# Optimization experiments

Measured on AMD Instinct MI355X. Metric: run time of the kernel, lower is better.

The kernel has to match this reference:

```python
import jax, jax.numpy as jnp
import numpy as np

BITS = 4
QMAX = (1 << BITS) - 1      # 15
QHALF = 1 << (BITS - 1)     # 8
B, S = 4, 2048
IN, OUT, FP = 4096, 4096, 256
INT = IN - FP


def setup_inputs() -> dict:
    key = jax.random.key(0)
    k0, k1, k2, k3 = jax.random.split(key, 4)
    x = jax.random.normal(k0, (B, S, IN), dtype=jnp.float16)
    # disjoint outlier / int feature index sets (QUIK splits columns by outlier-ness)
    perm = np.random.default_rng(0).permutation(IN)
    fp_indices = jnp.sort(jnp.asarray(perm[:FP], dtype=jnp.int32))
    int_indices = jnp.sort(jnp.asarray(perm[FP:], dtype=jnp.int32))
    # unpacked int4 weight values in [-8, 7] (torch stores these packed 2-per-uint8)
    int_weight = jax.random.randint(k1, (OUT, INT), -QHALF, QHALF, dtype=jnp.int8)
    weights_scales = (jax.random.uniform(k2, (OUT, 1), dtype=jnp.float32) * 0.01 + 1e-3).astype(jnp.float16)
    fp_weight = (jax.random.normal(k3, (OUT, FP), dtype=jnp.float32) * 0.02).astype(jnp.float16)
    bias = jnp.zeros((OUT,), dtype=jnp.float16)
    # reduced_w[j] = w_scale[j] * sum_k int_weight[j, k]  (precomputed zero-point correction)
    reduced_w = (weights_scales.astype(jnp.float32)[:, 0] * jnp.sum(int_weight.astype(jnp.float32), axis=1)).reshape(1, OUT).astype(jnp.float16)
    return {"x": x, "int_weight": int_weight, "fp_weight": fp_weight, "bias": bias,
            "weights_scales": weights_scales, "reduced_w": reduced_w,
            "int_indices": int_indices, "fp_indices": fp_indices}


def reference(x, int_weight, fp_weight, bias, weights_scales, reduced_w, int_indices, fp_indices):
    b, s, in_feat = x.shape
    xf = x.reshape(-1, in_feat)                       # [N, in] tokens
    int_x = xf[:, int_indices].astype(jnp.float32)    # [N, INT]
    fp_x = xf[:, fp_indices].astype(jnp.float32)      # [N, FP] outliers stay fp16-precision
    # asymmetric per-token quantization (quik.asymmetric.quantize)
    mn = jnp.min(int_x, axis=1, keepdims=True)
    mx = jnp.max(int_x, axis=1, keepdims=True)
    scale = jnp.maximum((mx - mn) / QMAX, 1e-8)       # [N,1]
    q = (jnp.clip(jnp.round((int_x - mn) / scale), 0, QMAX) - QHALF).astype(jnp.int8)  # signed int4 in [-8,7]
    zero = scale * QHALF + mn                         # [N,1] shifted zero point
    # int4 GEMM (quik.matmul.int4Matmul), int32 accumulate
    int_res = jnp.einsum('nk,ok->no', q, int_weight, preferred_element_type=jnp.int32)
    # fp outlier branch fused with bias (F.linear)
    fp_res = fp_x @ fp_weight.astype(jnp.float32).T + bias.astype(jnp.float32)[None, :]
    # quik.asymmetric.dequantize: q*scale_x*scale_w + zero_x*reduced_w + fp_result
    out = (int_res.astype(jnp.float32) * scale * weights_scales.astype(jnp.float32)[:, 0][None, :]
           + zero * reduced_w.astype(jnp.float32) + fp_res)
    return out.astype(jnp.float16).reshape(b, s, -1)
```

## Files before the change

kernel.cpp:

```cpp
#include <hip/hip_runtime.h>
#include <hip/hip_bf16.h>
#include <stdint.h>

#define N_TOK 8192
#define IN_F  4096
#define OUT_F 4096
#define FP_F  256
#define INT_F 3840
#define PROW  1920

typedef int    v4i   __attribute__((ext_vector_type(4)));
typedef int    v16i  __attribute__((ext_vector_type(16)));
typedef float  v16f  __attribute__((ext_vector_type(16)));
typedef __bf16 bf16x8 __attribute__((ext_vector_type(8)));

#define WS_QP   0u
#define WS_WP   15728640u
#define WS_FPX  23592960u
#define WS_WFP  27787264u
#define WS_F1   29884416u
#define WS_F2   29917184u
#define WS_F3   29949952u
#define WS_NEED 29982720u


__global__ __launch_bounds__(256) void zero_out_kernel(uint4* __restrict__ o) {
  o[(size_t)blockIdx.x * 256 + threadIdx.x] = uint4{0, 0, 0, 0};
}

__global__ __launch_bounds__(256) void pack_w_kernel(
    const int* __restrict__ w, uint8_t* __restrict__ wp) {
  int gid = blockIdx.x * 256 + threadIdx.x;
  int r = gid / 120, t = gid % 120;
  const int* src = w + (size_t)r * INT_F + t * 32;
  uint32_t u[4];
#pragma unroll
  for (int h = 0; h < 2; h++) {
    uint32_t a0 = 0, a1 = 0;
#pragma unroll
    for (int j = 0; j < 4; j++) {
      uint32_t lo0 = (uint32_t)(src[h * 16 + j] + 8) & 0xFu;
      uint32_t hi0 = (uint32_t)(src[h * 16 + 8 + j] + 8) & 0xFu;
      a0 |= (lo0 | (hi0 << 4)) << (8 * j);
      uint32_t lo1 = (uint32_t)(src[h * 16 + 4 + j] + 8) & 0xFu;
      uint32_t hi1 = (uint32_t)(src[h * 16 + 12 + j] + 8) & 0xFu;
      a1 |= (lo1 | (hi1 << 4)) << (8 * j);
    }
    u[h * 2] = a0; u[h * 2 + 1] = a1;
  }
  uint4 o4; o4.x = u[0]; o4.y = u[1]; o4.z = u[2]; o4.w = u[3];
  *(uint4*)(wp + (size_t)r * PROW + t * 16) = o4;
}

__global__ __launch_bounds__(256) void conv_wfp_kernel(
    const float* __restrict__ w, __hip_bfloat16* __restrict__ o) {
  int i = (blockIdx.x * 256 + threadIdx.x) * 4;
  float4 v = *(const float4*)(w + i);
  __hip_bfloat16 b[4] = {__float2bfloat16(v.x), __float2bfloat16(v.y),
                         __float2bfloat16(v.z), __float2bfloat16(v.w)};
  *(uint2*)(o + i) = *(const uint2*)b;
}

__global__ __launch_bounds__(256) void quant_kernel(
    const float* __restrict__ x,
    const int* __restrict__ int_idx, const int* __restrict__ fp_idx,
    uint8_t* __restrict__ qp, __hip_bfloat16* __restrict__ fpx,
    float* __restrict__ f1, float* __restrict__ f2, float* __restrict__ f3) {
  __shared__ float gath[INT_F];
  __shared__ float smn[4], smx[4], ssum[4];
  __shared__ float s_mn, s_sc;

  int n = blockIdx.x, tid = threadIdx.x;
  const float* xr = x + (size_t)n * IN_F;

  float lmn = 1e30f, lmx = -1e30f;
#pragma unroll
  for (int k = 0; k < 15; k++) {
    int i = tid + k * 256;
    float v = xr[int_idx[i]];
    int b = i >> 2;
    gath[(b ^ ((b >> 2) & 7)) * 4 + (i & 3)] = v;
    lmn = fminf(lmn, v);
    lmx = fmaxf(lmx, v);
  }
  fpx[(size_t)n * FP_F + tid] = __float2bfloat16(xr[fp_idx[tid]]);

#pragma unroll
  for (int off = 32; off > 0; off >>= 1) {
    lmn = fminf(lmn, __shfl_xor(lmn, off, 64));
    lmx = fmaxf(lmx, __shfl_xor(lmx, off, 64));
  }
  int wv = tid >> 6, ln = tid & 63;
  if (ln == 0) { smn[wv] = lmn; smx[wv] = lmx; }
  __syncthreads();
  if (tid == 0) {
    float mn = fminf(fminf(smn[0], smn[1]), fminf(smn[2], smn[3]));
    float mx = fmaxf(fmaxf(smx[0], smx[1]), fmaxf(smx[2], smx[3]));
    float sc = fmaxf((mx - mn) / 15.0f, 1e-8f);
    s_mn = mn; s_sc = sc;
    f1[n] = sc; f3[n] = mn;
  }
  __syncthreads();
  float mn = s_mn, sc = s_sc;

  float lsum = 0.0f;
  if (tid < 240) {
    int g = tid;
    const float4* g4 = (const float4*)gath;
    float4 q0 = g4[(g * 4 + 0) ^ (g & 7)];
    float4 q1 = g4[(g * 4 + 1) ^ (g & 7)];
    float4 q2 = g4[(g * 4 + 2) ^ (g & 7)];
    float4 q3 = g4[(g * 4 + 3) ^ (g & 7)];
    float vals[16] = {q0.x, q0.y, q0.z, q0.w, q1.x, q1.y, q1.z, q1.w,
                      q2.x, q2.y, q2.z, q2.w, q3.x, q3.y, q3.z, q3.w};
    uint32_t u0 = 0, u1 = 0;
#pragma unroll
    for (int i = 0; i < 4; i++) {
      float cA = fminf(fmaxf(rintf((vals[i] - mn) / sc), 0.0f), 15.0f);
      float cB = fminf(fmaxf(rintf((vals[i + 8] - mn) / sc), 0.0f), 15.0f);
      float cC = fminf(fmaxf(rintf((vals[i + 4] - mn) / sc), 0.0f), 15.0f);
      float cD = fminf(fmaxf(rintf((vals[i + 12] - mn) / sc), 0.0f), 15.0f);
      lsum += (cA + cB) + (cC + cD);
      u0 |= ((uint32_t)cA | ((uint32_t)cB << 4)) << (8 * i);
      u1 |= ((uint32_t)cC | ((uint32_t)cD << 4)) << (8 * i);
    }
    uint2 o2; o2.x = u0; o2.y = u1;
    *(uint2*)(qp + (size_t)n * PROW + g * 8) = o2;
  }
#pragma unroll
  for (int off = 32; off > 0; off >>= 1) lsum += __shfl_xor(lsum, off, 64);
  if (ln == 0) ssum[wv] = lsum;
  __syncthreads();
  if (tid == 0)
    f2[n] = -8.0f * (ssum[0] + ssum[1] + ssum[2] + ssum[3]) * s_sc;
}

__device__ inline v4i unpack_nib(uint2 u) {
  v4i r;
  r[0] = (int)(u.x & 0x0F0F0F0Fu);
  r[1] = (int)(u.y & 0x0F0F0F0Fu);
  r[2] = (int)((u.x >> 4) & 0x0F0F0F0Fu);
  r[3] = (int)((u.y >> 4) & 0x0F0F0F0Fu);
  return r;
}

__global__ __launch_bounds__(256, 4) void gemm_kernel(
    const uint8_t* __restrict__ qp, const uint8_t* __restrict__ wp,
    const __hip_bfloat16* __restrict__ fpx, const __hip_bfloat16* __restrict__ wfp,
    const float* __restrict__ f1, const float* __restrict__ f2,
    const float* __restrict__ f3,
    const float* __restrict__ wscale, const float* __restrict__ reduced,
    const float* __restrict__ bias, float* __restrict__ out) {
  __shared__ int4 lds4[1024];
  int8_t* lds = (int8_t*)lds4;

  int tid = threadIdx.x;
  int wave = tid >> 6, lane = tid & 63;
  int wm = wave >> 1, wn = wave & 1;
  int blk = blockIdx.x;
  int tileM = ((blk & 7) << 3) | ((blk >> 3) & 7);
  int tileN = blk >> 6;
  int n0 = tileM * 128, o0 = tileN * 128;

  union { v16i i; v16f f; } acc[2][2];
#pragma unroll
  for (int mi = 0; mi < 2; mi++)
#pragma unroll
    for (int ni = 0; ni < 2; ni++)
#pragma unroll
      for (int e = 0; e < 16; e++) acc[mi][ni].i[e] = 0;

  int m = lane & 31, kg = lane >> 5;
  int swm = (m & 3) ^ ((m >> 2) & 3);
  int sr = tid >> 1, sh = tid & 1;
  int swr = (sr & 3) ^ ((sr >> 2) & 3);
  uint32_t wa0 = (uint32_t)(sr * 4 + ((sh * 2) ^ swr)) * 8;
  uint32_t wa1 = (uint32_t)(sr * 4 + ((sh * 2 + 1) ^ swr)) * 8;
  const uint8_t* ga = qp + (size_t)(n0 + sr) * PROW + sh * 16;
  const uint8_t* gb = wp + (size_t)(o0 + sr) * PROW + sh * 16;

  uint4 pa = *(const uint4*)ga;
  uint4 pb = *(const uint4*)gb;
  for (int kt = 0; kt < 60; kt++) {
    {
      uint2 t0; t0.x = pa.x; t0.y = pa.y;
      uint2 t1; t1.x = pa.z; t1.y = pa.w;
      *(uint2*)&lds[wa0] = t0;
      *(uint2*)&lds[wa1] = t1;
      uint2 t2; t2.x = pb.x; t2.y = pb.y;
      uint2 t3; t3.x = pb.z; t3.y = pb.w;
      *(uint2*)&lds[4096 + wa0] = t2;
      *(uint2*)&lds[4096 + wa1] = t3;
    }
    __syncthreads();
    if (kt < 59) {
      pa = *(const uint4*)(ga + (kt + 1) * 32);
      pb = *(const uint4*)(gb + (kt + 1) * 32);
    }
#pragma unroll
    for (int ks = 0; ks < 2; ks++) {
      int slot = (ks * 2 + kg) ^ swm;
      v4i a[2], b[2];
#pragma unroll
      for (int mi = 0; mi < 2; mi++) {
        int row = wm * 64 + mi * 32 + m;
        a[mi] = unpack_nib(*(const uint2*)&lds[row * 32 + slot * 8]);
      }
#pragma unroll
      for (int ni = 0; ni < 2; ni++) {
        int row = wn * 64 + ni * 32 + m;
        b[ni] = unpack_nib(*(const uint2*)&lds[4096 + row * 32 + slot * 8]);
      }
#pragma unroll
      for (int mi = 0; mi < 2; mi++)
#pragma unroll
        for (int ni = 0; ni < 2; ni++)
          acc[mi][ni].i = __builtin_amdgcn_mfma_i32_32x32x32_i8(
              a[mi], b[ni], acc[mi][ni].i, 0, 0, 0);
    }
    __syncthreads();
  }

  int col = lane & 31, rb4 = (lane >> 5) * 4;
  float cws[2], crw[2], cbs[2];
#pragma unroll
  for (int ni = 0; ni < 2; ni++) {
    int o = o0 + wn * 64 + ni * 32 + col;
    cws[ni] = wscale[o]; crw[ni] = reduced[o]; cbs[ni] = bias[o];
  }
#pragma unroll
  for (int mi = 0; mi < 2; mi++) {
#pragma unroll
    for (int reg = 0; reg < 16; reg++) {
      int row = (reg & 3) + 8 * (reg >> 2) + rb4;
      int n = n0 + wm * 64 + mi * 32 + row;
      float a1 = f1[n], a2 = f2[n], a3 = f3[n];
      float d0 = (float)acc[mi][0].i[reg];
      float d1 = (float)acc[mi][1].i[reg];
      acc[mi][0].f[reg] = (d0 * a1 + a2) * cws[0] + a3 * crw[0] + cbs[0];
      acc[mi][1].f[reg] = (d1 * a1 + a2) * cws[1] + a3 * crw[1] + cbs[1];
    }
  }

  const int8_t* fpxb = (const int8_t*)fpx;
  const int8_t* fpwb = (const int8_t*)wfp;
  for (int kt = 0; kt < 8; kt++) {
#pragma unroll
    for (int i = 0; i < 2; i++) {
      int c = tid + i * 256;
      int r = c >> 2, s = c & 3;
      int ss = s ^ (r & 3) ^ ((r >> 2) & 3);
      *(int4*)&lds[(r * 4 + ss) * 16] =
          *(const int4*)(fpxb + (size_t)(n0 + r) * 512 + kt * 64 + s * 16);
    }
#pragma unroll
    for (int i = 0; i < 2; i++) {
      int c = tid + i * 256;
      int r = c >> 2, s = c & 3;
      int ss = s ^ (r & 3) ^ ((r >> 2) & 3);
      *(int4*)&lds[8192 + (r * 4 + ss) * 16] =
          *(const int4*)(fpwb + (size_t)(o0 + r) * 512 + kt * 64 + s * 16);
    }
    __syncthreads();
#pragma unroll
    for (int ks = 0; ks < 2; ks++) {
      bf16x8 a[2], b[2];
#pragma unroll
      for (int mi = 0; mi < 2; mi++) {
        int row = wm * 64 + mi * 32 + m;
        int seg = (ks * 2 + kg) ^ (row & 3) ^ ((row >> 2) & 3);
        a[mi] = *(const bf16x8*)&lds[(row * 4 + seg) * 16];
      }
#pragma unroll
      for (int ni = 0; ni < 2; ni++) {
        int row = wn * 64 + ni * 32 + m;
        int seg = (ks * 2 + kg) ^ (row & 3) ^ ((row >> 2) & 3);
        b[ni] = *(const bf16x8*)&lds[8192 + (row * 4 + seg) * 16];
      }
#pragma unroll
      for (int mi = 0; mi < 2; mi++)
#pragma unroll
        for (int ni = 0; ni < 2; ni++)
          acc[mi][ni].f = __builtin_amdgcn_mfma_f32_32x32x16_bf16(
              a[mi], b[ni], acc[mi][ni].f, 0, 0, 0);
    }
    __syncthreads();
  }

#pragma unroll
  for (int mi = 0; mi < 2; mi++) {
#pragma unroll
    for (int ni = 0; ni < 2; ni++) {
      int o = o0 + wn * 64 + ni * 32 + col;
#pragma unroll
      for (int reg = 0; reg < 16; reg++) {
        int row = (reg & 3) + 8 * (reg >> 2) + rb4;
        int n = n0 + wm * 64 + mi * 32 + row;
        out[(size_t)n * OUT_F + o] = acc[mi][ni].f[reg];
      }
    }
  }
}

extern "C" void kernel_launch(void* const* d_in, const int* in_sizes, int n_in,
                              void* d_out, int out_size, void* d_ws, size_t ws_size,
                              hipStream_t stream) {
  const float* x     = (const float*)d_in[0];
  const int*   int_w = (const int*)d_in[1];
  const float* fp_w  = (const float*)d_in[2];
  const float* bias  = (const float*)d_in[3];
  const float* wsc   = (const float*)d_in[4];
  const float* red   = (const float*)d_in[5];
  const int*   iidx  = (const int*)d_in[6];
  const int*   fidx  = (const int*)d_in[7];
  float*       out   = (float*)d_out;

  if (ws_size < (size_t)WS_NEED) {
    zero_out_kernel<<<out_size / 1024, 256, 0, stream>>>((uint4*)d_out);
    return;
  }

  uint8_t* ws = (uint8_t*)d_ws;
  uint8_t*        qp  = ws + WS_QP;
  uint8_t*        wpk = ws + WS_WP;
  __hip_bfloat16* fpx = (__hip_bfloat16*)(ws + WS_FPX);
  __hip_bfloat16* wfp = (__hip_bfloat16*)(ws + WS_WFP);
  float*          f1  = (float*)(ws + WS_F1);
  float*          f2  = (float*)(ws + WS_F2);
  float*          f3  = (float*)(ws + WS_F3);

  pack_w_kernel<<<OUT_F * 120 / 256, 256, 0, stream>>>(int_w, wpk);
  conv_wfp_kernel<<<OUT_F * FP_F / 4 / 256, 256, 0, stream>>>(fp_w, wfp);
  quant_kernel<<<N_TOK, 256, 0, stream>>>(x, iidx, fidx, qp, fpx, f1, f2, f3);
  gemm_kernel<<<(N_TOK / 128) * (OUT_F / 128), 256, 0, stream>>>(
      qp, wpk, fpx, wfp, f1, f2, f3, wsc, red, bias, out);
}
```

Measured before the change: 442.2 us.

## Double GEMM K-tile depth, coalesce weight packing, quantize in registers

The int4 GEMM main loop now stages 64 bytes of K per tile instead of 32, which halves the number of iterations and barriers. The fp outlier loop likewise moves 128-byte bf16 chunks, using a new XOR swizzle and twice the LDS. To fit the larger LDS footprint, launch bounds drop from 4 to 3 blocks per SM. The weight packing kernel now reads with vector int4 loads, one 32-bit output per thread. The quant kernel keeps the gathered values in registers, multiplies by a reciprocal instead of dividing, and packs nibbles through shuffles into a small LDS buffer before a coalesced store.

Result: faster. 414.7 us (-6.2%).

```diff
diff --git a/kernel.cpp b/kernel.cpp
--- a/kernel.cpp
+++ b/kernel.cpp
@@ -30,26 +30,16 @@
 
 __global__ __launch_bounds__(256) void pack_w_kernel(
     const int* __restrict__ w, uint8_t* __restrict__ wp) {
-  int gid = blockIdx.x * 256 + threadIdx.x;
-  int r = gid / 120, t = gid % 120;
-  const int* src = w + (size_t)r * INT_F + t * 32;
-  uint32_t u[4];
-#pragma unroll
-  for (int h = 0; h < 2; h++) {
-    uint32_t a0 = 0, a1 = 0;
-#pragma unroll
-    for (int j = 0; j < 4; j++) {
-      uint32_t lo0 = (uint32_t)(src[h * 16 + j] + 8) & 0xFu;
-      uint32_t hi0 = (uint32_t)(src[h * 16 + 8 + j] + 8) & 0xFu;
-      a0 |= (lo0 | (hi0 << 4)) << (8 * j);
-      uint32_t lo1 = (uint32_t)(src[h * 16 + 4 + j] + 8) & 0xFu;
-      uint32_t hi1 = (uint32_t)(src[h * 16 + 12 + j] + 8) & 0xFu;
-      a1 |= (lo1 | (hi1 << 4)) << (8 * j);
-    }
-    u[h * 2] = a0; u[h * 2 + 1] = a1;
-  }
-  uint4 o4; o4.x = u[0]; o4.y = u[1]; o4.z = u[2]; o4.w = u[3];
-  *(uint4*)(wp + (size_t)r * PROW + t * 16) = o4;
+  int t = blockIdx.x * 256 + threadIdx.x;
+  int r = t / 480, u = t % 480;
+  const int* src = w + (size_t)r * INT_F + (u >> 1) * 16 + (u & 1) * 4;
+  int4 lo = *(const int4*)src;
+  int4 hi = *(const int4*)(src + 8);
+  uint32_t o = (uint32_t)((lo.x + 8) & 15) | (uint32_t)((hi.x + 8) & 15) << 4 |
+               (uint32_t)((lo.y + 8) & 15) << 8 | (uint32_t)((hi.y + 8) & 15) << 12 |
+               (uint32_t)((lo.z + 8) & 15) << 16 | (uint32_t)((hi.z + 8) & 15) << 20 |
+               (uint32_t)((lo.w + 8) & 15) << 24 | (uint32_t)((hi.w + 8) & 15) << 28;
+  ((uint32_t*)wp)[t] = o;
 }
 
 __global__ __launch_bounds__(256) void conv_wfp_kernel(
@@ -66,22 +56,20 @@
     const int* __restrict__ int_idx, const int* __restrict__ fp_idx,
     uint8_t* __restrict__ qp, __hip_bfloat16* __restrict__ fpx,
     float* __restrict__ f1, float* __restrict__ f2, float* __restrict__ f3) {
-  __shared__ float gath[INT_F];
+  __shared__ uint2 qb[240];
   __shared__ float smn[4], smx[4], ssum[4];
-  __shared__ float s_mn, s_sc;
+  __shared__ float s_mn, s_inv, s_sc;
 
   int n = blockIdx.x, tid = threadIdx.x;
   const float* xr = x + (size_t)n * IN_F;
 
+  float v[15];
   float lmn = 1e30f, lmx = -1e30f;
 #pragma unroll
   for (int k = 0; k < 15; k++) {
-    int i = tid + k * 256;
-    float v = xr[int_idx[i]];
-    int b = i >> 2;
-    gath[(b ^ ((b >> 2) & 7)) * 4 + (i & 3)] = v;
-    lmn = fminf(lmn, v);
-    lmx = fmaxf(lmx, v);
+    v[k] = xr[int_idx[tid + 256 * k]];
+    lmn = fminf(lmn, v[k]);
+    lmx = fmaxf(lmx, v[k]);
   }
   fpx[(size_t)n * FP_F + tid] = __float2bfloat16(xr[fp_idx[tid]]);
 
@@ -97,35 +85,23 @@
     float mn = fminf(fminf(smn[0], smn[1]), fminf(smn[2], smn[3]));
     float mx = fmaxf(fmaxf(smx[0], smx[1]), fmaxf(smx[2], smx[3]));
     float sc = fmaxf((mx - mn) / 15.0f, 1e-8f);
-    s_mn = mn; s_sc = sc;
+    s_mn = mn; s_sc = sc; s_inv = 1.0f / sc;
     f1[n] = sc; f3[n] = mn;
   }
   __syncthreads();
-  float mn = s_mn, sc = s_sc;
-
+  float mn = s_mn, inv = s_inv;
+
+  uint8_t* qbb = (uint8_t*)qb;
   float lsum = 0.0f;
-  if (tid < 240) {
-    int g = tid;
-    const float4* g4 = (const float4*)gath;
-    float4 q0 = g4[(g * 4 + 0) ^ (g & 7)];
-    float4 q1 = g4[(g * 4 + 1) ^ (g & 7)];
-    float4 q2 = g4[(g * 4 + 2) ^ (g & 7)];
-    float4 q3 = g4[(g * 4 + 3) ^ (g & 7)];
-    float vals[16] = {q0.x, q0.y, q0.z, q0.w, q1.x, q1.y, q1.z, q1.w,
-                      q2.x, q2.y, q2.z, q2.w, q3.x, q3.y, q3.z, q3.w};
-    uint32_t u0 = 0, u1 = 0;
-#pragma unroll
-    for (int i = 0; i < 4; i++) {
-      float cA = fminf(fmaxf(rintf((vals[i] - mn) / sc), 0.0f), 15.0f);
-      float cB = fminf(fmaxf(rintf((vals[i + 8] - mn) / sc), 0.0f), 15.0f);
-      float cC = fminf(fmaxf(rintf((vals[i + 4] - mn) / sc), 0.0f), 15.0f);
-      float cD = fminf(fmaxf(rintf((vals[i + 12] - mn) / sc), 0.0f), 15.0f);
-      lsum += (cA + cB) + (cC + cD);
-      u0 |= ((uint32_t)cA | ((uint32_t)cB << 4)) << (8 * i);
-      u1 |= ((uint32_t)cC | ((uint32_t)cD << 4)) << (8 * i);
-    }
-    uint2 o2; o2.x = u0; o2.y = u1;
-    *(uint2*)(qp + (size_t)n * PROW + g * 8) = o2;
+#pragma unroll
+  for (int k = 0; k < 15; k++) {
+    float c = fminf(fmaxf(rintf((v[k] - mn) * inv), 0.0f), 15.0f);
+    lsum += c;
+    float ch = __shfl_down(c, 8, 64);
+    if ((tid & 15) < 8) {
+      qbb[(tid >> 4) * 8 + (tid & 7) + 128 * k] =
+          (uint8_t)((uint32_t)c | ((uint32_t)ch << 4));
+    }
   }
 #pragma unroll
   for (int off = 32; off > 0; off >>= 1) lsum += __shfl_xor(lsum, off, 64);
@@ -133,6 +109,8 @@
   __syncthreads();
   if (tid == 0)
     f2[n] = -8.0f * (ssum[0] + ssum[1] + ssum[2] + ssum[3]) * s_sc;
+  if (tid < 240)
+    *(uint2*)(qp + (size_t)n * PROW + tid * 8) = qb[tid];
 }
 
 __device__ inline v4i unpack_nib(uint2 u) {
@@ -144,14 +122,14 @@
   return r;
 }
 
-__global__ __launch_bounds__(256, 4) void gemm_kernel(
+__global__ __launch_bounds__(256, 3) void gemm_kernel(
     const uint8_t* __restrict__ qp, const uint8_t* __restrict__ wp,
     const __hip_bfloat16* __restrict__ fpx, const __hip_bfloat16* __restrict__ wfp,
     const float* __restrict__ f1, const float* __restrict__ f2,
     const float* __restrict__ f3,
     const float* __restrict__ wscale, const float* __restrict__ reduced,
     const float* __restrict__ bias, float* __restrict__ out) {
-  __shared__ int4 lds4[1024];
+  __shared__ int4 lds4[2048];
   int8_t* lds = (int8_t*)lds4;
 
   int tid = threadIdx.x;
@@ -171,45 +149,50 @@
       for (int e = 0; e < 16; e++) acc[mi][ni].i[e] = 0;
 
   int m = lane & 31, kg = lane >> 5;
-  int swm = (m & 3) ^ ((m >> 2) & 3);
-  int sr = tid >> 1, sh = tid & 1;
-  int swr = (sr & 3) ^ ((sr >> 2) & 3);
-  uint32_t wa0 = (uint32_t)(sr * 4 + ((sh * 2) ^ swr)) * 8;
-  uint32_t wa1 = (uint32_t)(sr * 4 + ((sh * 2 + 1) ^ swr)) * 8;
-  const uint8_t* ga = qp + (size_t)(n0 + sr) * PROW + sh * 16;
-  const uint8_t* gb = wp + (size_t)(o0 + sr) * PROW + sh * 16;
-
-  uint4 pa = *(const uint4*)ga;
-  uint4 pb = *(const uint4*)gb;
-  for (int kt = 0; kt < 60; kt++) {
+
+  int sra = tid >> 2, s16i = tid & 3;
+  const uint8_t* ga0 = qp + (size_t)(n0 + sra) * PROW + s16i * 16;
+  const uint8_t* ga1 = qp + (size_t)(n0 + sra + 64) * PROW + s16i * 16;
+  const uint8_t* gb0 = wp + (size_t)(o0 + sra) * PROW + s16i * 16;
+  const uint8_t* gb1 = wp + (size_t)(o0 + sra + 64) * PROW + s16i * 16;
+  uint32_t aw00 = sra * 64 + (((s16i * 2)     ^ ((sra >> 1) & 7)) * 8);
+  uint32_t aw01 = sra * 64 + (((s16i * 2 + 1) ^ ((sra >> 1) & 7)) * 8);
+  uint32_t aw10 = (sra + 64) * 64 + (((s16i * 2)     ^ (((sra + 64) >> 1) & 7)) * 8);
+  uint32_t aw11 = (sra + 64) * 64 + (((s16i * 2 + 1) ^ (((sra + 64) >> 1) & 7)) * 8);
+
+  uint4 pa0 = *(const uint4*)ga0, pa1 = *(const uint4*)ga1;
+  uint4 pb0 = *(const uint4*)gb0, pb1 = *(const uint4*)gb1;
+  for (int kt = 0; kt < 30; kt++) {
     {
-      uint2 t0; t0.x = pa.x; t0.y = pa.y;
-      uint2 t1; t1.x = pa.z; t1.y = pa.w;
-      *(uint2*)&lds[wa0] = t0;
-      *(uint2*)&lds[wa1] = t1;
-      uint2 t2; t2.x = pb.x; t2.y = pb.y;
-      uint2 t3; t3.x = pb.z; t3.y = pb.w;
-      *(uint2*)&lds[4096 + wa0] = t2;
-      *(uint2*)&lds[4096 + wa1] = t3;
+      uint2 t0; t0.x = pa0.x; t0.y = pa0.y; *(uint2*)&lds[aw00] = t0;
+      uint2 t1; t1.x = pa0.z; t1.y = pa0.w; *(uint2*)&lds[aw01] = t1;
+      uint2 t2; t2.x = pa1.x; t2.y = pa1.y; *(uint2*)&lds[aw10] = t2;
+      uint2 t3; t3.x = pa1.z; t3.y = pa1.w; *(uint2*)&lds[aw11] = t3;
+      uint2 t4; t4.x = pb0.x; t4.y = pb0.y; *(uint2*)&lds[8192 + aw00] = t4;
+      uint2 t5; t5.x = pb0.z; t5.y = pb0.w; *(uint2*)&lds[8192 + aw01] = t5;
+      uint2 t6; t6.x = pb1.x; t6.y = pb1.y; *(uint2*)&lds[8192 + aw10] = t6;
+      uint2 t7; t7.x = pb1.z; t7.y = pb1.w; *(uint2*)&lds[8192 + aw11] = t7;
     }
     __syncthreads();
-    if (kt < 59) {
-      pa = *(const uint4*)(ga + (kt + 1) * 32);
-      pb = *(const uint4*)(gb + (kt + 1) * 32);
-    }
-#pragma unroll
-    for (int ks = 0; ks < 2; ks++) {
-      int slot = (ks * 2 + kg) ^ swm;
+    if (kt < 29) {
+      pa0 = *(const uint4*)(ga0 + (kt + 1) * 64);
+      pa1 = *(const uint4*)(ga1 + (kt + 1) * 64);
+      pb0 = *(const uint4*)(gb0 + (kt + 1) * 64);
+      pb1 = *(const uint4*)(gb1 + (kt + 1) * 64);
+    }
+#pragma unroll
+    for (int ks = 0; ks < 4; ks++) {
+      int s8 = ks * 2 + kg;
       v4i a[2], b[2];
 #pragma unroll
       for (int mi = 0; mi < 2; mi++) {
         int row = wm * 64 + mi * 32 + m;
-        a[mi] = unpack_nib(*(const uint2*)&lds[row * 32 + slot * 8]);
+        a[mi] = unpack_nib(*(const uint2*)&lds[row * 64 + ((s8 ^ ((row >> 1) & 7)) * 8)]);
       }
 #pragma unroll
       for (int ni = 0; ni < 2; ni++) {
         int row = wn * 64 + ni * 32 + m;
-        b[ni] = unpack_nib(*(const uint2*)&lds[4096 + row * 32 + slot * 8]);
+        b[ni] = unpack_nib(*(const uint2*)&lds[8192 + row * 64 + ((s8 ^ ((row >> 1) & 7)) * 8)]);
       }
 #pragma unroll
       for (int mi = 0; mi < 2; mi++)
@@ -244,38 +227,31 @@
 
   const int8_t* fpxb = (const int8_t*)fpx;
   const int8_t* fpwb = (const int8_t*)wfp;
-  for (int kt = 0; kt < 8; kt++) {
-#pragma unroll
-    for (int i = 0; i < 2; i++) {
+  for (int kr = 0; kr < 4; kr++) {
+#pragma unroll
+    for (int i = 0; i < 4; i++) {
       int c = tid + i * 256;
-      int r = c >> 2, s = c & 3;
-      int ss = s ^ (r & 3) ^ ((r >> 2) & 3);
-      *(int4*)&lds[(r * 4 + ss) * 16] =
-          *(const int4*)(fpxb + (size_t)(n0 + r) * 512 + kt * 64 + s * 16);
-    }
-#pragma unroll
-    for (int i = 0; i < 2; i++) {
-      int c = tid + i * 256;
-      int r = c >> 2, s = c & 3;
-      int ss = s ^ (r & 3) ^ ((r >> 2) & 3);
-      *(int4*)&lds[8192 + (r * 4 + ss) * 16] =
-          *(const int4*)(fpwb + (size_t)(o0 + r) * 512 + kt * 64 + s * 16);
+      int row = c >> 3, s16 = c & 7;
+      int phys = s16 ^ ((row >> 1) & 7);
+      *(int4*)&lds[row * 128 + phys * 16] =
+          *(const int4*)(fpxb + (size_t)(n0 + row) * 512 + kr * 128 + s16 * 16);
+      *(int4*)&lds[16384 + row * 128 + phys * 16] =
+          *(const int4*)(fpwb + (size_t)(o0 + row) * 512 + kr * 128 + s16 * 16);
     }
     __syncthreads();
 #pragma unroll
-    for (int ks = 0; ks < 2; ks++) {
+    for (int kstep = 0; kstep < 4; kstep++) {
+      int s16 = kstep * 2 + kg;
       bf16x8 a[2], b[2];
 #pragma unroll
       for (int mi = 0; mi < 2; mi++) {
         int row = wm * 64 + mi * 32 + m;
-        int seg = (ks * 2 + kg) ^ (row & 3) ^ ((row >> 2) & 3);
-        a[mi] = *(const bf16x8*)&lds[(row * 4 + seg) * 16];
+        a[mi] = *(const bf16x8*)&lds[row * 128 + ((s16 ^ ((row >> 1) & 7)) * 16)];
       }
 #pragma unroll
       for (int ni = 0; ni < 2; ni++) {
         int row = wn * 64 + ni * 32 + m;
-        int seg = (ks * 2 + kg) ^ (row & 3) ^ ((row >> 2) & 3);
-        b[ni] = *(const bf16x8*)&lds[8192 + (row * 4 + seg) * 16];
+        b[ni] = *(const bf16x8*)&lds[16384 + row * 128 + ((s16 ^ ((row >> 1) & 7)) * 16)];
       }
 #pragma unroll
       for (int mi = 0; mi < 2; mi++)
@@ -329,7 +305,7 @@
   float*          f2  = (float*)(ws + WS_F2);
   float*          f3  = (float*)(ws + WS_F3);
 
-  pack_w_kernel<<<OUT_F * 120 / 256, 256, 0, stream>>>(int_w, wpk);
+  pack_w_kernel<<<OUT_F * 480 / 256, 256, 0, stream>>>(int_w, wpk);
   conv_wfp_kernel<<<OUT_F * FP_F / 4 / 256, 256, 0, stream>>>(fp_w, wfp);
   quant_kernel<<<N_TOK, 256, 0, stream>>>(x, iidx, fidx, qp, fpx, f1, f2, f3);
   gemm_kernel<<<(N_TOK / 128) * (OUT_F / 128), 256, 0, stream>>>(
```
